# Performance work log

Measured on AMD Instinct MI355X. Metric: run time of the kernel, lower is better.

Reference implementation:

```python
import jax, jax.numpy as jnp
import numpy as np

N_OBJS = 100          # max detections / scatter buffer size
TOP_K = 100           # top_k_n peaks per channel
KP_THRES = 0.3        # score threshold before NMS
NMS_IOU = 0.5
RESIZE_H, RESIZE_W = 1536.0, 1536.0   # resize_shape (== heatmap HxW here)
H, W = 1536, 1536


def _peak_hms(hms):
    # 3x3 stride-1 SAME max pool; keep only local maxima (Base.apply_max_pool)
    hmax = jax.lax.reduce_window(hms, -jnp.inf, jax.lax.max, (1, 3, 3, 1), (1, 1, 1, 1), 'SAME')
    return jnp.where(hms == hmax, hms, 0.0)


def _top_k_loc(hms, k):
    # per-channel top-k peak coordinates -> [b, c, k, 2] (y, x) int32
    b, h, w, c = hms.shape
    flat = jnp.transpose(hms, (0, 3, 1, 2)).reshape(b, c, h * w)
    _, idx = jax.lax.top_k(flat, k)
    return jnp.stack([idx // w, idx % w], axis=-1).astype(jnp.int32)


def _iou_matrix(boxes):
    # boxes [N,4] = (y1,x1,y2,x2)
    y1, x1, y2, x2 = boxes[:, 0], boxes[:, 1], boxes[:, 2], boxes[:, 3]
    area = jnp.maximum(y2 - y1, 0.0) * jnp.maximum(x2 - x1, 0.0)
    iy1 = jnp.maximum(y1[:, None], y1[None, :]); ix1 = jnp.maximum(x1[:, None], x1[None, :])
    iy2 = jnp.minimum(y2[:, None], y2[None, :]); ix2 = jnp.minimum(x2[:, None], x2[None, :])
    inter = jnp.maximum(iy2 - iy1, 0.0) * jnp.maximum(ix2 - ix1, 0.0)
    union = area[:, None] + area[None, :] - inter
    return inter / jnp.maximum(union, 1e-8)


def _nms_single(boxes, scores):
    # greedy single-class NMS, fixed-size (combined_non_max_suppression equivalent,
    # clip_boxes=False, score_threshold=-inf); padded slots are zeros like TF.
    order = jnp.argsort(-scores)
    boxes, scores = boxes[order], scores[order]
    n = boxes.shape[0]
    iou = _iou_matrix(boxes)
    idxs = jnp.arange(n)

    def step(suppressed, inp):
        i, iou_row = inp
        keep_i = ~suppressed[i]
        return suppressed | (keep_i & (iou_row > NMS_IOU) & (idxs > i)), keep_i

    _, keep = jax.lax.scan(step, jnp.zeros(n, bool), (idxs, iou))
    perm = jnp.argsort(jnp.where(keep, 0, 1))  # stable: compact kept to front, score order preserved
    keep_s = keep[perm]
    out_boxes = jnp.where(keep_s[:, None], boxes[perm], 0.0)
    out_scores = jnp.where(keep_s, scores[perm], 0.0)
    return out_boxes, out_scores, jnp.zeros(n, jnp.float32)


def _forward(obj_heat_map, offset_map, size_maps, origin_shapes):
    resize_shape = jnp.array([RESIZE_H, RESIZE_W], jnp.float32)
    ratio = origin_shapes / resize_shape                      # [b,2]
    hms = _peak_hms(obj_heat_map)                             # [b,H,W,2]
    b = hms.shape[0]
    coors = _top_k_loc(hms, TOP_K)                            # [b,2,K,2]
    b_coors, b_lnmks = coors[:, :1], coors[:, 1:]             # obj / nose coords
    bidx = jnp.arange(b)[:, None, None]

    # nose landmark: scores at nose-channel peaks, masked mean of coords (int mean like TF)
    nose_scores = hms[bidx, b_lnmks[..., 0], b_lnmks[..., 1], 1]     # [b,1,K]
    nose_mask = nose_scores > 0.5
    cnt = jnp.maximum(jnp.sum(nose_mask), 1)
    lnmk_mean = jnp.sum(jnp.where(nose_mask[..., None], b_lnmks, 0), axis=(0, 1, 2)) // cnt
    b_lnmks_m = lnmk_mean.reshape(b, 1, 2)                    # requires b == 1 (as in original)
    b_nose_scores = jnp.where(nose_mask, nose_scores, -1.0).reshape(b, -1)

    # boxes from sizes at object peaks
    size_vals = size_maps[bidx, b_coors[..., 0], b_coors[..., 1]]    # [b,1,K,2]
    obj_scores = hms[bidx, b_coors[..., 0], b_coors[..., 1], 0]      # [b,1,K]
    centers = b_coors.astype(jnp.float32)
    tls = jnp.maximum(centers - size_vals / 2.0, 0.0)
    brs = jnp.minimum(centers + size_vals / 2.0, resize_shape - 1.0)
    bboxes = jnp.concatenate([tls, brs], axis=-1) * jnp.tile(ratio, (1, 2))[:, None, None, :]
    bboxes, scores = bboxes[:, 0], obj_scores[:, 0]           # [b,K,4], [b,K]

    # scatter masked candidates into -1-initialized buffer (tensor_scatter_nd_update equivalent)
    mask = scores > KP_THRES
    cand = jnp.where(mask[..., None], jnp.concatenate([bboxes, scores[..., None]], -1), -1.0)
    cand = jnp.pad(cand, ((0, 0), (0, N_OBJS - TOP_K), (0, 0)), constant_values=-1.0)  # [b,N_OBJS,5]

    nb, ns, nc = jax.vmap(_nms_single)(cand[..., :4], cand[..., 4])
    box_results = jnp.where(nb == -1.0, jnp.inf, nb)
    box_results = jnp.where(box_results == 0.0, jnp.inf, box_results)  # (x - 1 == -1)
    b_bboxes = jnp.concatenate([box_results, ns[..., None], nc[..., None]], axis=-1)  # [b,N_OBJS,6]

    # offset vectors at the mean nose landmark (gather 8ch -> [b,n,4,2])
    bidx2 = jnp.arange(b)[:, None]
    off = offset_map[bidx2, b_lnmks_m[..., 0], b_lnmks_m[..., 1]].reshape(b, 1, 4, 2)
    lf = b_lnmks_m.astype(jnp.float32)
    b_ENM = (lf[:, :, None, :] - off) * ratio[:, None, None, :]
    b_lnmks_out = lf * ratio[:, None, :]
    return b_bboxes, b_lnmks_out, b_ENM, b_nose_scores


def setup_inputs() -> dict:
    key = jax.random.key(0)
    k1, k2, k3 = jax.random.split(key, 3)
    obj_heat_map = jax.random.uniform(k1, (1, H, W, 2), jnp.float32)
    offset_map = jax.random.normal(k2, (1, H, W, 8), jnp.float32) * 8.0
    size_maps = jax.random.uniform(k3, (1, H, W, 2), jnp.float32) * 128.0
    origin_shapes = jnp.array([[1080.0, 1920.0]], jnp.float32)
    return {"obj_heat_map": obj_heat_map, "offset_map": offset_map,
            "size_maps": size_maps, "origin_shapes": origin_shapes}


def reference(obj_heat_map, offset_map, size_maps, origin_shapes):
    return _forward(obj_heat_map, offset_map, size_maps, origin_shapes)
```

## Files before the change

kernel.cpp:

```cpp
#include <hip/hip_runtime.h>
#include <cstdint>

#define IW 1536
#define IH 1536
#define TOPK 100
#define CAPB 128
#define CAPT 8192
#define BF_INF16 0x7F7Fu

#define NBLK 192
#define VBTOT 576
#define LTCAP 1024

typedef unsigned u32; typedef unsigned long long u64; typedef unsigned short u16;

#define OH1   0
#define OCNT  4096
#define OSEL  4102
#define OLSD  4106
#define OBAR  4170
#define OZEND 4176
#define OSCR  4176
#define OLB   (OSCR + 2*CAPT + 2)
#define OLT   (OLB + 4*CAPB)

__device__ __forceinline__ u32 enc16(u32 b){ b &= 0xFFFFu; return (b & 0x8000u) ? ((~b)&0xFFFFu) : (b|0x8000u); }
__device__ __forceinline__ u32 dec16(u32 e){ return (e & 0x8000u) ? (e^0x8000u) : ((~e)&0xFFFFu); }
__device__ __forceinline__ float up16(u32 b){ return __uint_as_float((b&0xFFFFu)<<16); }
__device__ __forceinline__ u16 f2bf(float f){ u32 u=__float_as_uint(f); return (u16)((u + 0x7FFFu + ((u>>16)&1u))>>16); }

__device__ __forceinline__ void wave_sel2048(const u32* bins, u32 need, int* Dout, u32* Aout){
  int lane = threadIdx.x & 63;
  u32 s = 0;
  #pragma unroll
  for(int k=0;k<32;++k) s += bins[lane*32+k];
  u32 c = s;
  #pragma unroll
  for(int off=1;off<64;off<<=1){
    u32 v = __shfl_down(c, off, 64);
    if(lane + off < 64) c += v;
  }
  u32 cnext = __shfl_down(c, 1, 64); if(lane==63) cnext = 0u;
  u64 m = __ballot(c >= need);
  if(m == 0ull){ if(lane==0){ *Dout = 0; *Aout = 0u; } return; }
  int L = 63 - __builtin_clzll((unsigned long long)m);
  if(lane == L){
    u32 above = cnext; int D = 32*L;
    for(int b=32*L+31; b>=32*L; --b){
      u32 h = bins[b];
      if(above + h >= need){ D = b; break; }
      above += h;
    }
    *Dout = D; *Aout = above;
  }
}

union SMem {
  struct {
    u32 lh[4096];
    u32 lsdl[64];
    u64 bbuf[2][CAPB];
    u64 tbuf[2][LTCAP];
  } ab;
  struct {
    u32 h2s[2048];
    u64 keysS[CAPB];
    u32 selS[CAPB];
    u32 wbitsS[64];
    u32 lsdS[32];
    u32 hdr[10];
    float val[TOPK]; int vidx[TOPK];
    float cbox[TOPK][4]; float cscore[TOPK]; float area[TOPK];
    int sup[TOPK]; int slotv[TOPK];
    u64 nbits[2*TOPK];
  } c;
};

__device__ __forceinline__ void grid_arrive(u32* ctr){
  __hip_atomic_fetch_add(ctr, 1u, __ATOMIC_RELEASE, __HIP_MEMORY_SCOPE_AGENT);
}
__device__ __forceinline__ void grid_wait(u32* ctr, u32 target){
  while(__hip_atomic_load(ctr, __ATOMIC_ACQUIRE, __HIP_MEMORY_SCOPE_AGENT) < target)
    __builtin_amdgcn_s_sleep(2);
}

__global__ __launch_bounds__(1024, 4) void fused_kernel(
    const u32* __restrict__ hm, u32* __restrict__ ws,
    const u32* __restrict__ szm, const u16* __restrict__ offm,
    const u16* __restrict__ orig, u16* __restrict__ out){
  __shared__ SMem S;
  __shared__ int Dsh[2]; __shared__ u32 Ash[2];
  __shared__ u32 bcntS[2], tcntS[2], bbaseS[2], tbaseS[2];
  __shared__ int selcS, selc2S, BvS, LshS, tcS;
  __shared__ u64 suppS[2];
  __shared__ int cS, srS, scS;

  int tid = threadIdx.x, lane = tid & 63;

  for(int i=tid;i<4096;i+=1024) S.ab.lh[i]=0u;
  __syncthreads();
  for(int vb = blockIdx.x; vb < VBTOT; vb += NBLK){
    int p = (vb*1024 + tid)*4;
    int y = p / IW, x = p - y*IW;
    const u32* R1 = hm + y*IW;
    const u32* R0 = y ? R1 - IW : R1;
    const u32* R2 = (y < IH-1) ? R1 + IW : R1;
    uint4 c0 = *(const uint4*)(R0+x), c1 = *(const uint4*)(R1+x), c2 = *(const uint4*)(R2+x);
    int xl = x ? x-1 : 0, xr = (x+4 < IW) ? x+4 : IW-1;
    u32 a0[6] = {R0[xl], c0.x, c0.y, c0.z, c0.w, R0[xr]};
    u32 a1[6] = {R1[xl], c1.x, c1.y, c1.z, c1.w, R1[xr]};
    u32 a2[6] = {R2[xl], c2.x, c2.y, c2.z, c2.w, R2[xr]};

    #pragma unroll
    for(int j=0;j<4;++j){
      u32 cc = a1[j+1];
      u32 cl = cc & 0xFFFFu, chv = cc >> 16;
      u32 m0=0u, m1=0u;
      #pragma unroll
      for(int d=0;d<3;++d){
        u32 n0=a0[j+d], n2=a2[j+d]; u32 t;
        t=n0&0xFFFFu; m0=t>m0?t:m0;  t=n0>>16; m1=t>m1?t:m1;
        t=n2&0xFFFFu; m0=t>m0?t:m0;  t=n2>>16; m1=t>m1?t:m1;
      }
      { u32 n=a1[j];   u32 t=n&0xFFFFu; m0=t>m0?t:m0; t=n>>16; m1=t>m1?t:m1; }
      { u32 n=a1[j+2]; u32 t=n&0xFFFFu; m0=t>m0?t:m0; t=n>>16; m1=t>m1?t:m1; }
      if(cl  >= m0) atomicAdd(&S.ab.lh[enc16(cl)>>5], 1u);
      if(chv >= m1) atomicAdd(&S.ab.lh[2048 + (enc16(chv)>>5)], 1u);
    }
  }
  __syncthreads();
  for(int i=tid;i<4096;i+=1024) if(S.ab.lh[i]) atomicAdd(&ws[OH1+i], S.ab.lh[i]);

  __syncthreads();
  if(tid==0){ grid_arrive(&ws[OBAR]); grid_wait(&ws[OBAR], (u32)NBLK); }
  __syncthreads();

  for(int i=tid;i<4096;i+=1024) S.ab.lh[i] = ws[OH1+i];
  if(tid < 64) S.ab.lsdl[tid] = 0u;
  if(tid < 2){ bcntS[tid] = 0u; tcntS[tid] = 0u; }
  __syncthreads();
  if(tid < 64)       wave_sel2048(S.ab.lh,        (u32)TOPK, &Dsh[0], &Ash[0]);
  else if(tid < 128) wave_sel2048(S.ab.lh + 2048, (u32)TOPK, &Dsh[1], &Ash[1]);
  __syncthreads();
  if(blockIdx.x == 0 && tid < 2){ ws[OSEL+tid] = (u32)Dsh[tid]; ws[OSEL+2+tid] = Ash[tid]; }

  {
    u32 thrD0 = (u32)Dsh[0] << 5, thrD1 = (u32)Dsh[1] << 5;
    u64* listBw = (u64*)(ws + OLB);
    u64* tieW   = (u64*)(ws + OLT);
    for(int vb = blockIdx.x; vb < VBTOT; vb += NBLK){
      int p = (vb*1024 + tid)*4;
      int y = p / IW, x = p - y*IW;
      const u32* R1 = hm + y*IW;
      uint4 c1v = *(const uint4*)(R1+x);
      u32 cen[4] = {c1v.x, c1v.y, c1v.z, c1v.w};
      const u32* R0 = y ? R1 - IW : R1;
      const u32* R2 = (y < IH-1) ? R1 + IW : R1;
      #pragma unroll
      for(int j=0;j<4;++j){
        u32 cc = cen[j];
        u32 cl = cc & 0xFFFFu, chv = cc >> 16;
        u32 e0 = enc16(cl), e1 = enc16(chv);
        bool cand0 = (e0 >= thrD0), cand1 = (e1 >= thrD1);
        if(!(cand0 || cand1)) continue;
        int xx = x + j;
        int xm = xx ? xx-1 : 0, xp = (xx+1 < IW) ? xx+1 : IW-1;
        u32 n0a=R0[xm], n0b=R0[xx], n0c=R0[xp];
        u32 n1a=R1[xm],             n1c=R1[xp];
        u32 n2a=R2[xm], n2b=R2[xx], n2c=R2[xp];
        u32 m0=0u, m1=0u, t;
        t=n0a&0xFFFFu; m0=t>m0?t:m0;  t=n0a>>16; m1=t>m1?t:m1;
        t=n0b&0xFFFFu; m0=t>m0?t:m0;  t=n0b>>16; m1=t>m1?t:m1;
        t=n0c&0xFFFFu; m0=t>m0?t:m0;  t=n0c>>16; m1=t>m1?t:m1;
        t=n1a&0xFFFFu; m0=t>m0?t:m0;  t=n1a>>16; m1=t>m1?t:m1;
        t=n1c&0xFFFFu; m0=t>m0?t:m0;  t=n1c>>16; m1=t>m1?t:m1;
        t=n2a&0xFFFFu; m0=t>m0?t:m0;  t=n2a>>16; m1=t>m1?t:m1;
        t=n2b&0xFFFFu; m0=t>m0?t:m0;  t=n2b>>16; m1=t>m1?t:m1;
        t=n2c&0xFFFFu; m0=t>m0?t:m0;  t=n2c>>16; m1=t>m1?t:m1;
        u32 idx = (u32)(p + j);
        u64 key0 = ((u64)e0<<32) | (u32)(~idx);
        u64 key1 = ((u64)e1<<32) | (u32)(~idx);
        if(cand0 && cl >= m0){
          if((e0>>5) > (u32)Dsh[0]){
            u32 pos = atomicAdd(&bcntS[0], 1u);
            if(pos < CAPB) S.ab.bbuf[0][pos] = key0;
          } else {
            u32 pos = atomicAdd(&tcntS[0], 1u);
            if(pos < LTCAP) S.ab.tbuf[0][pos] = key0;
            else { u32 g = atomicAdd(&ws[OCNT+4], 1u); if(g < CAPT) tieW[g] = key0; }
            atomicAdd(&S.ab.lsdl[e0 & 31u], 1u);
          }
        }
        if(cand1 && chv >= m1){
          if((e1>>5) > (u32)Dsh[1]){
            u32 pos = atomicAdd(&bcntS[1], 1u);
            if(pos < CAPB) S.ab.bbuf[1][pos] = key1;
          } else {
            u32 pos = atomicAdd(&tcntS[1], 1u);
            if(pos < LTCAP) S.ab.tbuf[1][pos] = key1;
            else { u32 g = atomicAdd(&ws[OCNT+5], 1u); if(g < CAPT) tieW[CAPT + g] = key1; }
            atomicAdd(&S.ab.lsdl[32 + (e1 & 31u)], 1u);
          }
        }
      }
    }
    __syncthreads();
    if(tid < 64 && S.ab.lsdl[tid]) atomicAdd(&ws[OLSD + tid], S.ab.lsdl[tid]);
    if(tid < 2){
      u32 n = bcntS[tid]; if(n > CAPB) n = CAPB;
      bcntS[tid] = n;
      bbaseS[tid] = n ? atomicAdd(&ws[OCNT+2+tid], n) : 0u;
    } else if(tid < 4){
      int ch2 = tid - 2;
      u32 n = tcntS[ch2]; if(n > LTCAP) n = LTCAP;
      tcntS[ch2] = n;
      tbaseS[ch2] = n ? atomicAdd(&ws[OCNT+4+ch2], n) : 0u;
    }
    __syncthreads();
    for(int ch2=0; ch2<2; ++ch2){
      u32 n = bcntS[ch2], base = bbaseS[ch2];
      for(u32 i=tid;i<n;i+=1024){
        u32 g = base + i;
        if(g < CAPB) listBw[ch2*CAPB + g] = S.ab.bbuf[ch2][i];
      }
      n = tcntS[ch2]; base = tbaseS[ch2];
      for(u32 i=tid;i<n;i+=1024){
        u32 g = base + i;
        if(g < CAPT) tieW[ch2*CAPT + g] = S.ab.tbuf[ch2][i];
      }
    }
  }

  __syncthreads();
  if(tid==0) grid_arrive(&ws[OBAR+1]);
  if(blockIdx.x >= 2) return;
  if(tid==0) grid_wait(&ws[OBAR+1], (u32)NBLK);
  __syncthreads();

  {
    int ch = (int)blockIdx.x;

    if(tid < 10) S.c.hdr[tid] = ws[OCNT + tid];
    if(tid < 32) S.c.lsdS[tid] = ws[OLSD + ch*32 + tid];
    for(int i=tid;i<2048;i+=1024) S.c.h2s[i] = 0u;
    if(tid < 64) S.c.wbitsS[tid] = 0u;
    if(tid == 0){ selcS = 0; selc2S = 0; BvS = 0; LshS = 0; tcS = 0; }
    if(tid < TOPK){ S.c.val[tid]=0.0f; S.c.vidx[tid]=0; }
    __syncthreads();

    int nB = (int)S.c.hdr[2+ch]; if(nB > CAPB) nB = CAPB;
    int nT = (int)S.c.hdr[4+ch]; if(nT > CAPT) nT = CAPT;
    int D  = (int)S.c.hdr[6+ch];
    u32 above = S.c.hdr[8+ch];
    const u64* listB = ((const u64*)(ws + OLB)) + ch*CAPB;
    const u64* tie   = ((const u64*)(ws + OLT)) + ch*CAPT;
    u32* tidxG = ws + OSCR + ch*CAPT;

    if(tid < 64){
      u32 h = (lane < 32) ? S.c.lsdS[lane] : 0u;
      u32 c = h;
      #pragma unroll
      for(int off=1;off<32;off<<=1){
        u32 v = __shfl_down(c, off, 64);
        if(lane + off < 32) c += v;
      }
      u32 need2 = (u32)TOPK - above;
      u64 m = __ballot(lane >= 1 && lane < 32 && c >= need2);
      if(lane == 0){
        LshS = m ? (63 - __builtin_clzll((unsigned long long)m)) : 0;
        selcS = nB;
      }
    }
    for(int i=tid;i<nB;i+=1024) S.c.keysS[i] = listB[i];
    __syncthreads();
    u32 thr = ((u32)D<<5) | (u32)LshS;
    float tval = up16(dec16(thr));

    for(int base2=0; base2<nT; base2+=1024){
      int i = base2 + tid;
      bool act = (i < nT);
      u64 k = 0; u32 e = 0, idx = 0;
      if(act){ k = tie[i]; e = (u32)(k>>32); idx = ~(u32)(k & 0xFFFFFFFFu); }
      if(act && e > thr){
        int pos = atomicAdd(&selcS, 1); if(pos < CAPB) S.c.keysS[pos] = k;
      }
      bool isT = act && (e == thr);
      u64 mk = __ballot(isT);
      if(mk){
        u32 cw = __popcll(mk), b;
        if(lane==0) b = (u32)atomicAdd(&tcS, (int)cw);
        b = __shfl(b, 0);
        if(isT){
          u32 pos = b + __popcll(mk & ((1ull<<lane)-1ull));
          if(pos < CAPT) tidxG[pos] = idx;
        }
      }
      if(isT) atomicAdd(&S.c.h2s[idx>>11], 1u);
    }
    __syncthreads();

    int nA = selcS; if(nA > CAPB) nA = CAPB; if(nA > TOPK) nA = TOPK;
    int need = TOPK - nA;
    if(tid < nA){
      u64 kreg = S.c.keysS[tid];
      int r = 0;
      for(int j=0;j<nA;++j) r += (S.c.keysS[j] > kreg);
      if(r < TOPK){
        S.c.val[r] = up16(dec16((u32)(kreg>>32)));
        S.c.vidx[r] = (int)(~(u32)(kreg & 0xFFFFFFFFu));
      }
    }
    if(tid < 64){
      const u32* hh = S.c.h2s;
      int base = lane*32;
      u32 s = 0;
      #pragma unroll
      for(int k2=0;k2<32;++k2) s += hh[base+k2];
      u32 c = s;
      #pragma unroll
      for(int off=1;off<64;off<<=1){
        u32 v = __shfl_up(c, off, 64);
        if(lane >= off) c += v;
      }
      u64 m = __ballot(need > 0 && c >= (u32)need);
      int L = m ? (int)(__ffsll((unsigned long long)m) - 1) : -1;
      if(L >= 0 && lane == L){
        u32 hb[32];
        #pragma unroll
        for(int k2=0;k2<32;++k2) hb[k2] = hh[base+k2];
        u32 cum2 = c - s;
        int Bsel = base;
        #pragma unroll
        for(int k2=0;k2<32;++k2){
          if(cum2 + hb[k2] >= (u32)need){ Bsel = base+k2; break; }
          cum2 += hb[k2];
        }
        BvS = Bsel;
      }
    }
    __syncthreads();

    int B = BvS;
    int tc = tcS; if(tc > CAPT) tc = CAPT;
    if(need > 0){
      for(int i=tid;i<tc;i+=1024){
        u32 idx = tidxG[i];
        int b = (int)(idx>>11);
        if(b < B){
          int pos = atomicAdd(&selc2S, 1);
          if(pos < CAPB) S.c.selS[pos] = idx;
        } else if(b == B){
          atomicOr(&S.c.wbitsS[(idx&2047)>>5], 1u<<(idx&31));
        }
      }
    }
    __syncthreads();

    int sc = selc2S; if(sc > CAPB) sc = CAPB;
    if(need > 0 && tid < sc){
      u32 v = S.c.selS[tid];
      int r = 0;
      for(int j=0;j<sc;++j) r += (S.c.selS[j] < v);
      if(nA + r < TOPK){ S.c.val[nA+r] = tval; S.c.vidx[nA+r] = (int)v; }
    }
    if(need > 0 && tid < 64){
      u32 bits = S.c.wbitsS[tid];
      u32 cnt = __popc(bits);
      u32 incl = cnt;
      #pragma unroll
      for(int off=1;off<64;off<<=1){
        u32 v = __shfl_up(incl, off, 64);
        if(lane >= off) incl += v;
      }
      int excl = (int)(incl - cnt);
      int rem = need - sc;
      int pos = nA + sc + excl;
      int j = 0;
      while(bits){
        int l = __ffs(bits) - 1; bits &= bits - 1;
        if(excl + j < rem && pos + j < TOPK){
          S.c.val[pos+j] = tval;
          S.c.vidx[pos+j] = (int)(((u32)B<<11) | ((u32)tid<<5) | (u32)l);
        }
        ++j;
      }
    }
    __syncthreads();

    float ry = up16(orig[0]) / 1536.0f;
    float rx = up16(orig[1]) / 1536.0f;

    if(ch == 1){
      if(tid == 0){ cS = 0; srS = 0; scS = 0; }
      __syncthreads();
      if(tid < TOPK && S.c.val[tid] > 0.5f){
        atomicAdd(&cS, 1);
        atomicAdd(&srS, S.c.vidx[tid] / IW);
        atomicAdd(&scS, S.c.vidx[tid] % IW);
      }
      if(tid < TOPK) out[610 + tid] = f2bf(S.c.val[tid] > 0.5f ? S.c.val[tid] : -1.0f);
      __syncthreads();
      if(tid == 0){
        int c = cS < 1 ? 1 : cS;
        int meanr = srS / c, meanc = scS / c;
        float lfy = (float)meanr, lfx = (float)meanc;
        out[600] = f2bf(lfy * ry);
        out[601] = f2bf(lfx * rx);
        const u16* op = offm + ((size_t)meanr*IW + meanc)*8;
        for(int p=0;p<4;++p){
          out[602 + p*2 + 0] = f2bf((lfy - up16(op[p*2+0])) * ry);
          out[602 + p*2 + 1] = f2bf((lfx - up16(op[p*2+1])) * rx);
        }
      }
      return;
    }

    if(tid < TOPK){
      int idx = S.c.vidx[tid];
      int r = idx / IW, c = idx - r*IW;
      float score = S.c.val[tid];
      u32 sz = szm[idx];
      float sy = up16(sz), sx = up16(sz>>16);
      float cy = (float)r, cx = (float)c;
      float tly = fmaxf(cy - sy*0.5f, 0.0f);
      float tlx = fmaxf(cx - sx*0.5f, 0.0f);
      float bry = fminf(cy + sy*0.5f, 1535.0f);
      float brx = fminf(cx + sx*0.5f, 1535.0f);
      bool mk = score > 0.3f;
      float b0 = mk ? tly*ry : -1.0f;
      float b1 = mk ? tlx*rx : -1.0f;
      float b2 = mk ? bry*ry : -1.0f;
      float b3 = mk ? brx*rx : -1.0f;
      S.c.cbox[tid][0]=b0; S.c.cbox[tid][1]=b1; S.c.cbox[tid][2]=b2; S.c.cbox[tid][3]=b3;
      S.c.cscore[tid] = mk ? score : -1.0f;
      S.c.area[tid] = fmaxf(b2-b0,0.0f) * fmaxf(b3-b1,0.0f);
    }
    if(tid < 2*TOPK) S.c.nbits[tid] = 0ull;
    __syncthreads();

    for(int t=tid; t<TOPK*TOPK; t+=1024){
      int i = t / TOPK, j = t - i*TOPK;
      if(j > i){
        float iy1 = fmaxf(S.c.cbox[i][0], S.c.cbox[j][0]);
        float ix1 = fmaxf(S.c.cbox[i][1], S.c.cbox[j][1]);
        float iy2 = fminf(S.c.cbox[i][2], S.c.cbox[j][2]);
        float ix2 = fminf(S.c.cbox[i][3], S.c.cbox[j][3]);
        float inter = fmaxf(iy2-iy1,0.0f) * fmaxf(ix2-ix1,0.0f);
        float uni = (S.c.area[i] + S.c.area[j]) - inter;
        if(inter / fmaxf(uni, 1e-8f) > 0.5f)
          atomicOr(&S.c.nbits[i*2 + (j>>6)], 1ull << (j&63));
      }
    }
    __syncthreads();
    if(tid == 0){
      u64 s0 = 0ull, s1 = 0ull;
      for(int base=0;base<TOPK;base+=10){
        u64 buf[20];
        #pragma unroll
        for(int k=0;k<20;++k) buf[k] = S.c.nbits[2*base+k];
        #pragma unroll
        for(int k=0;k<10;++k){
          int i = base+k;
          bool su = (i<64) ? ((s0>>i)&1ull) : ((s1>>(i-64))&1ull);
          if(!su){ s0 |= buf[2*k]; s1 |= buf[2*k+1]; }
        }
      }
      suppS[0] = s0; suppS[1] = s1;
    }
    __syncthreads();
    if(tid < TOPK) S.c.sup[tid] = (int)((suppS[tid>>6] >> (tid&63)) & 1ull);
    __syncthreads();

    if(tid < TOPK){
      int kbefore = 0, sbefore = 0, ktot = 0;
      for(int j=0;j<TOPK;++j){
        int sj = S.c.sup[j];
        ktot += (1 - sj);
        if(j < tid){ kbefore += (1 - sj); sbefore += sj; }
      }
      int slot = S.c.sup[tid] ? (ktot + sbefore) : kbefore;
      S.c.slotv[slot] = tid;
    }
    __syncthreads();

    if(tid < TOPK){
      int s = S.c.slotv[tid];
      bool ks = !S.c.sup[s];
      u16 row[6];
      if(ks){
        for(int d=0;d<4;++d){
          float v = S.c.cbox[s][d];
          row[d] = (v == -1.0f || v == 0.0f) ? (u16)BF_INF16 : f2bf(v);
        }
        row[4] = f2bf(S.c.cscore[s]);
      } else {
        for(int d=0;d<4;++d) row[d] = (u16)BF_INF16;
        row[4] = 0;
      }
      row[5] = 0;
      for(int d=0;d<6;++d) out[tid*6 + d] = row[d];
    }
  }
}

extern "C" void kernel_launch(void* const* d_in, const int* in_sizes, int n_in,
                              void* d_out, int out_size, void* d_ws, size_t ws_size,
                              hipStream_t stream) {
  const u32* heat = (const u32*)d_in[0];
  const u16* offm = (const u16*)d_in[1];
  const u32* szm  = (const u32*)d_in[2];
  const u16* orig = (const u16*)d_in[3];
  u16* out = (u16*)d_out;
  u32* ws = (u32*)d_ws;

  hipMemsetAsync(ws, 0, OZEND*sizeof(u32), stream);
  fused_kernel<<<NBLK, 1024, 0, stream>>>(heat, ws, szm, offm, orig, out);
}
```

Before: 168.7 us.

## Shard global histograms, counters and barriers into segments; use packed u16 max

Splits the global histogram, candidate counters, tie lists and grid-barrier counters into four segments keyed by block index. This reduces same-address atomic contention across the 192 blocks, and the readers now sum the four segments. The 3x3 max pool now uses v_pk_max_u16 on packed bf16 pairs and gets horizontal neighbours through lane shuffles instead of extra loads. The low-digit tie histogram is rebuilt in the final blocks from the tie lists rather than with global atomics. The occupancy hint in launch_bounds is dropped, and the final stage now does more serial reading.

Result: slower. 186.4 us (+10.5%).

```diff
diff --git a/kernel.cpp b/kernel.cpp
--- a/kernel.cpp
+++ b/kernel.cpp
@@ -6,6 +6,8 @@
 #define TOPK 100
 #define CAPB 128
 #define CAPT 8192
+#define SEGT 8192
+#define NSEG 4
 #define BF_INF16 0x7F7Fu
 
 #define NBLK 192
@@ -15,19 +17,22 @@
 typedef unsigned u32; typedef unsigned long long u64; typedef unsigned short u16;
 
 #define OH1   0
-#define OCNT  4096
-#define OSEL  4102
-#define OLSD  4106
-#define OBAR  4170
-#define OZEND 4176
-#define OSCR  4176
-#define OLB   (OSCR + 2*CAPT + 2)
-#define OLT   (OLB + 4*CAPB)
+#define OCNTB (NSEG*4096)
+#define OCNTT (OCNTB + NSEG*2)
+#define OBAR  (OCNTT + NSEG*2)
+#define OZEND (OBAR + 2*NSEG)
+#define OSCR  OZEND
+#define OLB   (OSCR + 2*CAPT)
+#define OLT   (OLB + NSEG*2*CAPB*2)
 
 __device__ __forceinline__ u32 enc16(u32 b){ b &= 0xFFFFu; return (b & 0x8000u) ? ((~b)&0xFFFFu) : (b|0x8000u); }
 __device__ __forceinline__ u32 dec16(u32 e){ return (e & 0x8000u) ? (e^0x8000u) : ((~e)&0xFFFFu); }
 __device__ __forceinline__ float up16(u32 b){ return __uint_as_float((b&0xFFFFu)<<16); }
 __device__ __forceinline__ u16 f2bf(float f){ u32 u=__float_as_uint(f); return (u16)((u + 0x7FFFu + ((u>>16)&1u))>>16); }
+
+__device__ __forceinline__ u32 pkmaxu16(u32 a, u32 b){
+  u32 d; asm("v_pk_max_u16 %0, %1, %2" : "=v"(d) : "v"(a), "v"(b)); return d;
+}
 
 __device__ __forceinline__ void wave_sel2048(const u32* bins, u32 need, int* Dout, u32* Aout){
   int lane = threadIdx.x & 63;
@@ -58,7 +63,6 @@
 union SMem {
   struct {
     u32 lh[4096];
-    u32 lsdl[64];
     u64 bbuf[2][CAPB];
     u64 tbuf[2][LTCAP];
   } ab;
@@ -68,7 +72,7 @@
     u32 selS[CAPB];
     u32 wbitsS[64];
     u32 lsdS[32];
-    u32 hdr[10];
+    u32 cB[NSEG]; u32 cT[NSEG];
     float val[TOPK]; int vidx[TOPK];
     float cbox[TOPK][4]; float cscore[TOPK]; float area[TOPK];
     int sup[TOPK]; int slotv[TOPK];
@@ -76,86 +80,95 @@
   } c;
 };
 
-__device__ __forceinline__ void grid_arrive(u32* ctr){
-  __hip_atomic_fetch_add(ctr, 1u, __ATOMIC_RELEASE, __HIP_MEMORY_SCOPE_AGENT);
+__device__ __forceinline__ void grid_arrive(u32* base, u32 seg){
+  __hip_atomic_fetch_add(base + seg, 1u, __ATOMIC_RELEASE, __HIP_MEMORY_SCOPE_AGENT);
 }
-__device__ __forceinline__ void grid_wait(u32* ctr, u32 target){
-  while(__hip_atomic_load(ctr, __ATOMIC_ACQUIRE, __HIP_MEMORY_SCOPE_AGENT) < target)
+__device__ __forceinline__ void grid_wait_sum(u32* base, u32 target){
+  for(;;){
+    u32 s = 0;
+    #pragma unroll
+    for(int r=0;r<NSEG;++r) s += __hip_atomic_load(base + r, __ATOMIC_ACQUIRE, __HIP_MEMORY_SCOPE_AGENT);
+    if(s >= target) break;
     __builtin_amdgcn_s_sleep(2);
+  }
 }
 
-__global__ __launch_bounds__(1024, 4) void fused_kernel(
+__global__ __launch_bounds__(1024) void fused_kernel(
     const u32* __restrict__ hm, u32* __restrict__ ws,
     const u32* __restrict__ szm, const u16* __restrict__ offm,
     const u16* __restrict__ orig, u16* __restrict__ out){
   __shared__ SMem S;
   __shared__ int Dsh[2]; __shared__ u32 Ash[2];
-  __shared__ u32 bcntS[2], tcntS[2], bbaseS[2], tbaseS[2];
+  __shared__ u32 bcnt[2], tcnt[2], bbase[2], tbase[2];
   __shared__ int selcS, selc2S, BvS, LshS, tcS;
   __shared__ u64 suppS[2];
   __shared__ int cS, srS, scS;
 
   int tid = threadIdx.x, lane = tid & 63;
+  u32 seg = (u32)blockIdx.x & (NSEG-1);
 
   for(int i=tid;i<4096;i+=1024) S.ab.lh[i]=0u;
   __syncthreads();
   for(int vb = blockIdx.x; vb < VBTOT; vb += NBLK){
     int p = (vb*1024 + tid)*4;
     int y = p / IW, x = p - y*IW;
-    const u32* R1 = hm + y*IW;
-    const u32* R0 = y ? R1 - IW : R1;
-    const u32* R2 = (y < IH-1) ? R1 + IW : R1;
-    uint4 c0 = *(const uint4*)(R0+x), c1 = *(const uint4*)(R1+x), c2 = *(const uint4*)(R2+x);
-    int xl = x ? x-1 : 0, xr = (x+4 < IW) ? x+4 : IW-1;
-    u32 a0[6] = {R0[xl], c0.x, c0.y, c0.z, c0.w, R0[xr]};
-    u32 a1[6] = {R1[xl], c1.x, c1.y, c1.z, c1.w, R1[xr]};
-    u32 a2[6] = {R2[xl], c2.x, c2.y, c2.z, c2.w, R2[xr]};
-
+    const u32* P1 = hm + y*IW;
+    const u32* P0 = y ? P1 - IW : P1;
+    const u32* P2 = (y < IH-1) ? P1 + IW : P1;
+    uint4 c0 = *(const uint4*)(P0+x), c1 = *(const uint4*)(P1+x), c2 = *(const uint4*)(P2+x);
+    u32 L0 = __shfl_up(c0.w,1,64), L1 = __shfl_up(c1.w,1,64), L2 = __shfl_up(c2.w,1,64);
+    if(lane==0){ int xl = x ? x-1 : 0; L0=P0[xl]; L1=P1[xl]; L2=P2[xl]; }
+    u32 T0 = __shfl_down(c0.x,1,64), T1 = __shfl_down(c1.x,1,64), T2 = __shfl_down(c2.x,1,64);
+    if(lane==63){ int xr = (x+4 < IW) ? x+4 : IW-1; T0=P0[xr]; T1=P1[xr]; T2=P2[xr]; }
+    u32 a0[6] = {L0, c0.x, c0.y, c0.z, c0.w, T0};
+    u32 a1[6] = {L1, c1.x, c1.y, c1.z, c1.w, T1};
+    u32 a2[6] = {L2, c2.x, c2.y, c2.z, c2.w, T2};
+    u32 v[6], w[6];
+    #pragma unroll
+    for(int k=0;k<6;++k){ w[k] = pkmaxu16(a0[k], a2[k]); v[k] = pkmaxu16(w[k], a1[k]); }
     #pragma unroll
     for(int j=0;j<4;++j){
+      u32 m = pkmaxu16(pkmaxu16(v[j], w[j+1]), v[j+2]);
       u32 cc = a1[j+1];
-      u32 cl = cc & 0xFFFFu, chv = cc >> 16;
-      u32 m0=0u, m1=0u;
-      #pragma unroll
-      for(int d=0;d<3;++d){
-        u32 n0=a0[j+d], n2=a2[j+d]; u32 t;
-        t=n0&0xFFFFu; m0=t>m0?t:m0;  t=n0>>16; m1=t>m1?t:m1;
-        t=n2&0xFFFFu; m0=t>m0?t:m0;  t=n2>>16; m1=t>m1?t:m1;
-      }
-      { u32 n=a1[j];   u32 t=n&0xFFFFu; m0=t>m0?t:m0; t=n>>16; m1=t>m1?t:m1; }
-      { u32 n=a1[j+2]; u32 t=n&0xFFFFu; m0=t>m0?t:m0; t=n>>16; m1=t>m1?t:m1; }
-      if(cl  >= m0) atomicAdd(&S.ab.lh[enc16(cl)>>5], 1u);
-      if(chv >= m1) atomicAdd(&S.ab.lh[2048 + (enc16(chv)>>5)], 1u);
-    }
-  }
-  __syncthreads();
-  for(int i=tid;i<4096;i+=1024) if(S.ab.lh[i]) atomicAdd(&ws[OH1+i], S.ab.lh[i]);
-
-  __syncthreads();
-  if(tid==0){ grid_arrive(&ws[OBAR]); grid_wait(&ws[OBAR], (u32)NBLK); }
-  __syncthreads();
-
-  for(int i=tid;i<4096;i+=1024) S.ab.lh[i] = ws[OH1+i];
-  if(tid < 64) S.ab.lsdl[tid] = 0u;
-  if(tid < 2){ bcntS[tid] = 0u; tcntS[tid] = 0u; }
+      u32 cl = cc & 0xFFFFu, ch = cc >> 16;
+      if(cl >= (m & 0xFFFFu)) atomicAdd(&S.ab.lh[enc16(cl)>>5], 1u);
+      if(ch >= (m >> 16))     atomicAdd(&S.ab.lh[2048 + (enc16(ch)>>5)], 1u);
+    }
+  }
+  __syncthreads();
+  {
+    u32 rot = ((u32)blockIdx.x * 97u) & 4095u;
+    u32* H = ws + OH1 + seg*4096;
+    for(int i=tid;i<4096;i+=1024){
+      u32 b = ((u32)i + rot) & 4095u;
+      if(S.ab.lh[b]) atomicAdd(&H[b], S.ab.lh[b]);
+    }
+  }
+
+  __syncthreads();
+  if(tid==0){ grid_arrive(ws+OBAR, seg); grid_wait_sum(ws+OBAR, (u32)NBLK); }
+  __syncthreads();
+
+  for(int i=tid;i<4096;i+=1024)
+    S.ab.lh[i] = ws[OH1+i] + ws[OH1+4096+i] + ws[OH1+8192+i] + ws[OH1+12288+i];
+  if(tid < 2){ bcnt[tid]=0u; tcnt[tid]=0u; }
   __syncthreads();
   if(tid < 64)       wave_sel2048(S.ab.lh,        (u32)TOPK, &Dsh[0], &Ash[0]);
   else if(tid < 128) wave_sel2048(S.ab.lh + 2048, (u32)TOPK, &Dsh[1], &Ash[1]);
   __syncthreads();
-  if(blockIdx.x == 0 && tid < 2){ ws[OSEL+tid] = (u32)Dsh[tid]; ws[OSEL+2+tid] = Ash[tid]; }
 
   {
     u32 thrD0 = (u32)Dsh[0] << 5, thrD1 = (u32)Dsh[1] << 5;
-    u64* listBw = (u64*)(ws + OLB);
-    u64* tieW   = (u64*)(ws + OLT);
+    u64* tieSeg0 = ((u64*)(ws + OLT)) + (seg*2+0)*SEGT;
+    u64* tieSeg1 = ((u64*)(ws + OLT)) + (seg*2+1)*SEGT;
     for(int vb = blockIdx.x; vb < VBTOT; vb += NBLK){
       int p = (vb*1024 + tid)*4;
       int y = p / IW, x = p - y*IW;
-      const u32* R1 = hm + y*IW;
-      uint4 c1v = *(const uint4*)(R1+x);
+      const u32* P1 = hm + y*IW;
+      uint4 c1v = *(const uint4*)(P1+x);
       u32 cen[4] = {c1v.x, c1v.y, c1v.z, c1v.w};
-      const u32* R0 = y ? R1 - IW : R1;
-      const u32* R2 = (y < IH-1) ? R1 + IW : R1;
+      const u32* P0 = y ? P1 - IW : P1;
+      const u32* P2 = (y < IH-1) ? P1 + IW : P1;
       #pragma unroll
       for(int j=0;j<4;++j){
         u32 cc = cen[j];
@@ -165,9 +178,9 @@
         if(!(cand0 || cand1)) continue;
         int xx = x + j;
         int xm = xx ? xx-1 : 0, xp = (xx+1 < IW) ? xx+1 : IW-1;
-        u32 n0a=R0[xm], n0b=R0[xx], n0c=R0[xp];
-        u32 n1a=R1[xm],             n1c=R1[xp];
-        u32 n2a=R2[xm], n2b=R2[xx], n2c=R2[xp];
+        u32 n0a=P0[xm], n0b=P0[xx], n0c=P0[xp];
+        u32 n1a=P1[xm],             n1c=P1[xp];
+        u32 n2a=P2[xm], n2b=P2[xx], n2c=P2[xp];
         u32 m0=0u, m1=0u, t;
         t=n0a&0xFFFFu; m0=t>m0?t:m0;  t=n0a>>16; m1=t>m1?t:m1;
         t=n0b&0xFFFFu; m0=t>m0?t:m0;  t=n0b>>16; m1=t>m1?t:m1;
@@ -182,79 +195,89 @@
         u64 key1 = ((u64)e1<<32) | (u32)(~idx);
         if(cand0 && cl >= m0){
           if((e0>>5) > (u32)Dsh[0]){
-            u32 pos = atomicAdd(&bcntS[0], 1u);
+            u32 pos = atomicAdd(&bcnt[0], 1u);
             if(pos < CAPB) S.ab.bbuf[0][pos] = key0;
           } else {
-            u32 pos = atomicAdd(&tcntS[0], 1u);
+            u32 pos = atomicAdd(&tcnt[0], 1u);
             if(pos < LTCAP) S.ab.tbuf[0][pos] = key0;
-            else { u32 g = atomicAdd(&ws[OCNT+4], 1u); if(g < CAPT) tieW[g] = key0; }
-            atomicAdd(&S.ab.lsdl[e0 & 31u], 1u);
+            else { u32 g = atomicAdd(&ws[OCNTT + seg*2 + 0], 1u); if(g < SEGT) tieSeg0[g] = key0; }
           }
         }
         if(cand1 && chv >= m1){
           if((e1>>5) > (u32)Dsh[1]){
-            u32 pos = atomicAdd(&bcntS[1], 1u);
+            u32 pos = atomicAdd(&bcnt[1], 1u);
             if(pos < CAPB) S.ab.bbuf[1][pos] = key1;
           } else {
-            u32 pos = atomicAdd(&tcntS[1], 1u);
+            u32 pos = atomicAdd(&tcnt[1], 1u);
             if(pos < LTCAP) S.ab.tbuf[1][pos] = key1;
-            else { u32 g = atomicAdd(&ws[OCNT+5], 1u); if(g < CAPT) tieW[CAPT + g] = key1; }
-            atomicAdd(&S.ab.lsdl[32 + (e1 & 31u)], 1u);
+            else { u32 g = atomicAdd(&ws[OCNTT + seg*2 + 1], 1u); if(g < SEGT) tieSeg1[g] = key1; }
           }
         }
       }
     }
-    __syncthreads();
-    if(tid < 64 && S.ab.lsdl[tid]) atomicAdd(&ws[OLSD + tid], S.ab.lsdl[tid]);
-    if(tid < 2){
-      u32 n = bcntS[tid]; if(n > CAPB) n = CAPB;
-      bcntS[tid] = n;
-      bbaseS[tid] = n ? atomicAdd(&ws[OCNT+2+tid], n) : 0u;
-    } else if(tid < 4){
-      int ch2 = tid - 2;
-      u32 n = tcntS[ch2]; if(n > LTCAP) n = LTCAP;
-      tcntS[ch2] = n;
-      tbaseS[ch2] = n ? atomicAdd(&ws[OCNT+4+ch2], n) : 0u;
-    }
-    __syncthreads();
-    for(int ch2=0; ch2<2; ++ch2){
-      u32 n = bcntS[ch2], base = bbaseS[ch2];
-      for(u32 i=tid;i<n;i+=1024){
-        u32 g = base + i;
-        if(g < CAPB) listBw[ch2*CAPB + g] = S.ab.bbuf[ch2][i];
-      }
-      n = tcntS[ch2]; base = tbaseS[ch2];
-      for(u32 i=tid;i<n;i+=1024){
-        u32 g = base + i;
-        if(g < CAPT) tieW[ch2*CAPT + g] = S.ab.tbuf[ch2][i];
-      }
-    }
-  }
-
-  __syncthreads();
-  if(tid==0) grid_arrive(&ws[OBAR+1]);
+  }
+  __syncthreads();
+  if(tid < 2){
+    u32 n = bcnt[tid]; if(n > CAPB) n = CAPB;
+    bcnt[tid] = n;
+    bbase[tid] = n ? atomicAdd(&ws[OCNTB + seg*2 + tid], n) : 0u;
+  } else if(tid < 4){
+    int ch2 = tid - 2;
+    u32 n = tcnt[ch2]; if(n > LTCAP) n = LTCAP;
+    tcnt[ch2] = n;
+    tbase[ch2] = n ? atomicAdd(&ws[OCNTT + seg*2 + ch2], n) : 0u;
+  }
+  __syncthreads();
+  for(int ch2=0; ch2<2; ++ch2){
+    u64* listBw = ((u64*)(ws + OLB)) + (seg*2+ch2)*CAPB;
+    u64* tieW   = ((u64*)(ws + OLT)) + (seg*2+ch2)*SEGT;
+    u32 n = bcnt[ch2], base = bbase[ch2];
+    for(u32 i=tid;i<n;i+=1024){ u32 g = base + i; if(g < CAPB) listBw[g] = S.ab.bbuf[ch2][i]; }
+    n = tcnt[ch2]; base = tbase[ch2];
+    for(u32 i=tid;i<n;i+=1024){ u32 g = base + i; if(g < SEGT) tieW[g] = S.ab.tbuf[ch2][i]; }
+  }
+
+  __syncthreads();
+  if(tid==0) grid_arrive(ws+OBAR+NSEG, seg);
   if(blockIdx.x >= 2) return;
-  if(tid==0) grid_wait(&ws[OBAR+1], (u32)NBLK);
+  if(tid==0) grid_wait_sum(ws+OBAR+NSEG, (u32)NBLK);
   __syncthreads();
 
   {
     int ch = (int)blockIdx.x;
 
-    if(tid < 10) S.c.hdr[tid] = ws[OCNT + tid];
-    if(tid < 32) S.c.lsdS[tid] = ws[OLSD + ch*32 + tid];
+    if(tid < NSEG){ u32 v = ws[OCNTB + tid*2 + ch]; S.c.cB[tid] = v > CAPB ? CAPB : v; }
+    else if(tid < 2*NSEG){ int s = tid-NSEG; u32 v = ws[OCNTT + s*2 + ch]; S.c.cT[s] = v > SEGT ? SEGT : v; }
     for(int i=tid;i<2048;i+=1024) S.c.h2s[i] = 0u;
-    if(tid < 64) S.c.wbitsS[tid] = 0u;
+    if(tid >= 64 && tid < 128) S.c.wbitsS[tid-64] = 0u;
+    if(tid >= 128 && tid < 160) S.c.lsdS[tid-128] = 0u;
     if(tid == 0){ selcS = 0; selc2S = 0; BvS = 0; LshS = 0; tcS = 0; }
-    if(tid < TOPK){ S.c.val[tid]=0.0f; S.c.vidx[tid]=0; }
-    __syncthreads();
-
-    int nB = (int)S.c.hdr[2+ch]; if(nB > CAPB) nB = CAPB;
-    int nT = (int)S.c.hdr[4+ch]; if(nT > CAPT) nT = CAPT;
-    int D  = (int)S.c.hdr[6+ch];
-    u32 above = S.c.hdr[8+ch];
-    const u64* listB = ((const u64*)(ws + OLB)) + ch*CAPB;
-    const u64* tie   = ((const u64*)(ws + OLT)) + ch*CAPT;
+    if(tid >= 160 && tid < 160+TOPK){ S.c.val[tid-160]=0.0f; S.c.vidx[tid-160]=0; }
+    __syncthreads();
+
+    int D  = Dsh[ch];
+    u32 above = Ash[ch];
+    int nB = (int)(S.c.cB[0]+S.c.cB[1]+S.c.cB[2]+S.c.cB[3]); if(nB > CAPB) nB = CAPB;
     u32* tidxG = ws + OSCR + ch*CAPT;
+
+    {
+      u32 ob = 0;
+      for(int s2=0;s2<NSEG;++s2){
+        const u64* Lp = ((const u64*)(ws + OLB)) + (s2*2+ch)*CAPB;
+        u32 n = S.c.cB[s2];
+        for(u32 i=tid;i<n;i+=1024){ u32 g = ob+i; if(g < CAPB) S.c.keysS[g] = Lp[i]; }
+        ob += n;
+      }
+      for(int s2=0;s2<NSEG;++s2){
+        const u64* Tp = ((const u64*)(ws + OLT)) + (s2*2+ch)*SEGT;
+        u32 n = S.c.cT[s2];
+        for(u32 i=tid;i<n;i+=1024){
+          u32 e = (u32)(Tp[i] >> 32);
+          atomicAdd(&S.c.lsdS[e & 31u], 1u);
+        }
+      }
+    }
+    __syncthreads();
 
     if(tid < 64){
       u32 h = (lane < 32) ? S.c.lsdS[lane] : 0u;
@@ -271,31 +294,34 @@
         selcS = nB;
       }
     }
-    for(int i=tid;i<nB;i+=1024) S.c.keysS[i] = listB[i];
     __syncthreads();
     u32 thr = ((u32)D<<5) | (u32)LshS;
     float tval = up16(dec16(thr));
 
-    for(int base2=0; base2<nT; base2+=1024){
-      int i = base2 + tid;
-      bool act = (i < nT);
-      u64 k = 0; u32 e = 0, idx = 0;
-      if(act){ k = tie[i]; e = (u32)(k>>32); idx = ~(u32)(k & 0xFFFFFFFFu); }
-      if(act && e > thr){
-        int pos = atomicAdd(&selcS, 1); if(pos < CAPB) S.c.keysS[pos] = k;
-      }
-      bool isT = act && (e == thr);
-      u64 mk = __ballot(isT);
-      if(mk){
-        u32 cw = __popcll(mk), b;
-        if(lane==0) b = (u32)atomicAdd(&tcS, (int)cw);
-        b = __shfl(b, 0);
-        if(isT){
-          u32 pos = b + __popcll(mk & ((1ull<<lane)-1ull));
-          if(pos < CAPT) tidxG[pos] = idx;
-        }
-      }
-      if(isT) atomicAdd(&S.c.h2s[idx>>11], 1u);
+    for(int s2=0;s2<NSEG;++s2){
+      const u64* tie = ((const u64*)(ws + OLT)) + (s2*2+ch)*SEGT;
+      int nTs = (int)S.c.cT[s2];
+      for(int base2=0; base2<nTs; base2+=1024){
+        int i = base2 + tid;
+        bool act = (i < nTs);
+        u64 k = 0; u32 e = 0, idx = 0;
+        if(act){ k = tie[i]; e = (u32)(k>>32); idx = ~(u32)(k & 0xFFFFFFFFu); }
+        if(act && e > thr){
+          int pos = atomicAdd(&selcS, 1); if(pos < CAPB) S.c.keysS[pos] = k;
+        }
+        bool isT = act && (e == thr);
+        u64 mk = __ballot(isT);
+        if(mk){
+          u32 cw = __popcll(mk), b;
+          if(lane==0) b = (u32)atomicAdd(&tcS, (int)cw);
+          b = __shfl(b, 0);
+          if(isT){
+            u32 pos = b + __popcll(mk & ((1ull<<lane)-1ull));
+            if(pos < CAPT) tidxG[pos] = idx;
+          }
+        }
+        if(isT) atomicAdd(&S.c.h2s[idx>>11], 1u);
+      }
     }
     __syncthreads();
 
```
